# Kernel tuning notes

Measured on AMD Instinct MI355X. Metric: run time of the kernel, lower is better.

Reference implementation:

```python
import jax, jax.numpy as jnp
import numpy as np

NUM_CATEGORIES = 64
INPUT_DIM = 256
HIDDEN_DIM = 256
N = 4096  # number of samples (each with its own category)
M = 16    # rows per sample


def setup_inputs() -> dict:
    key = jax.random.key(0)
    k_x, k_cat, k_W = jax.random.split(key, 3)
    x = jax.random.normal(k_x, (N, M, INPUT_DIM), dtype=jnp.float32)
    cat_ids = jax.random.randint(k_cat, (N,), 0, NUM_CATEGORIES, dtype=jnp.int64)
    W = 0.02 * jax.random.normal(k_W, (NUM_CATEGORIES, INPUT_DIM, HIDDEN_DIM), dtype=jnp.float32)
    b = jnp.zeros((NUM_CATEGORIES, HIDDEN_DIM), dtype=jnp.float32)
    return {"x": x, "cat_ids": cat_ids, "W": W, "b": b}


def reference(x, cat_ids, W, b):
    # Gather per-sample weights/biases, then batched matmul + bias add.
    selected_W = W[cat_ids]              # [N, input_dim, hidden_dim]
    selected_b = b[cat_ids]              # [N, hidden_dim]
    out = jnp.einsum('nmi,nih->nmh', x, selected_W) + selected_b[:, None, :]
    return out
```

## Files before the change

kernel.cpp:

```cpp
#include <hip/hip_runtime.h>
#include <hip/hip_bf16.h>
#include <stdint.h>

#define N_SAMPLES 4096
#define M_ROWS 16
#define K_DIM 256
#define H_DIM 256
#define N_CATS 64
#define SPB 4
#define MAX_PADDED (N_SAMPLES + N_CATS * (SPB - 1))
#define NGROUP (MAX_PADDED / SPB)
#define GPX (NGROUP / 8)
#define GEMM_GRID (NGROUP * 2)
#define AROW 264

typedef _Float16 half8 __attribute__((ext_vector_type(8)));
typedef _Float16 half4 __attribute__((ext_vector_type(4)));
typedef float floatx4 __attribute__((ext_vector_type(4)));

#define WT_BYTES ((size_t)N_CATS * K_DIM * H_DIM * 2)
#define GCAT_OFF WT_BYTES
#define ORD_OFF  (WT_BYTES + 4288)
#define WS_NEED  (ORD_OFF + (size_t)MAX_PADDED * 4)

__global__ __launch_bounds__(256)
void prep_combined(const float* __restrict__ W, _Float16* __restrict__ Wt,
                   const int* __restrict__ cat, int* __restrict__ ord,
                   int* __restrict__ gcat) {
  const int tid = threadIdx.x;
  if (blockIdx.x < 1024) {
    __shared__ _Float16 t[64][72];
    const int bid = blockIdx.x;
    const int c  = bid >> 4;
    const int kb = (bid >> 2) & 3;
    const int hb = bid & 3;
    const int r  = tid >> 2;
    const int cg = (tid & 3) * 16;
    const float* src = W + ((size_t)c << 16) + (size_t)(kb * 64 + r) * 256 + hb * 64 + cg;
#pragma unroll
    for (int j = 0; j < 16; j += 4) {
      float4 v = *(const float4*)(src + j);
      t[r][cg + j + 0] = (_Float16)v.x;
      t[r][cg + j + 1] = (_Float16)v.y;
      t[r][cg + j + 2] = (_Float16)v.z;
      t[r][cg + j + 3] = (_Float16)v.w;
    }
    __syncthreads();
    _Float16* dst = Wt + ((size_t)c << 16) + (size_t)(hb * 64 + r) * 256 + kb * 64 + cg;
    half8 o0, o1;
#pragma unroll
    for (int j = 0; j < 8; j++) o0[j] = t[cg + j][r];
#pragma unroll
    for (int j = 0; j < 8; j++) o1[j] = t[cg + 8 + j][r];
    *(half8*)(dst) = o0;
    *(half8*)(dst + 8) = o1;
  } else {
    __shared__ int hist[N_CATS];
    __shared__ int poffs[N_CATS];
    __shared__ int curs[N_CATS];
    if (tid < N_CATS) hist[tid] = 0;
    for (int i = tid; i < MAX_PADDED; i += 256) ord[i] = -1;
    for (int i = tid; i < NGROUP; i += 256) gcat[i] = 0;
    __syncthreads();
    for (int i = tid; i < N_SAMPLES; i += 256) atomicAdd(&hist[cat[i]], 1);
    __syncthreads();
    if (tid == 0) {
      int run = 0;
      for (int c = 0; c < N_CATS; c++) {
        poffs[c] = run;
        run += ((hist[c] + SPB - 1) / SPB) * SPB;
      }
    }
    if (tid < N_CATS) curs[tid] = 0;
    __syncthreads();
    if (tid < N_CATS) {
      const int c = tid;
      const int g0 = poffs[c] >> 2;
      const int ng = (hist[c] + SPB - 1) >> 2;
      for (int g = 0; g < ng; g++) gcat[g0 + g] = c;
    }
    for (int i = tid; i < N_SAMPLES; i += 256) {
      int c = cat[i];
      int p = poffs[c] + atomicAdd(&curs[c], 1);
      ord[p] = i;
    }
  }
}

__global__ __launch_bounds__(256, 4)
void gemm_kernel(const float* __restrict__ x, const float* __restrict__ bias,
                 const _Float16* __restrict__ Wt, const int* __restrict__ ord,
                 const int* __restrict__ gcat, float* __restrict__ out) {
  __shared__ __align__(16) _Float16 sA[64 * AROW];

  const int tid = threadIdx.x;
  const int B = blockIdx.x;
  const int xcd = B & 7;
  const int slot = B >> 3;
  const int h_half = slot & 1;
  const int group = xcd * GPX + (slot >> 1);
  const int h0 = h_half << 7;

  const int cat = gcat[group];
  const int4 sm = *(const int4*)(ord + group * 4);
  if (sm.x < 0) return;

  const int wid  = tid >> 6;
  const int lane = tid & 63;
  const int l15  = lane & 15;
  const int quad = lane >> 4;

  const _Float16* wbase = Wt + ((size_t)cat << 16);

  half8 bf[8][2];
#pragma unroll
  for (int kt = 0; kt < 4; kt++)
#pragma unroll
    for (int nt = 0; nt < 2; nt++) {
      const int col = h0 + wid * 32 + nt * 16 + l15;
      bf[kt][nt] = *(const half8*)(wbase + (size_t)col * K_DIM + kt * 32 + quad * 8);
    }
  __builtin_amdgcn_sched_barrier(0);

  const int smp = (wid == 0) ? sm.x : (wid == 1) ? sm.y : (wid == 2) ? sm.z : sm.w;
  const float* asrc = (smp >= 0) ? (x + ((size_t)smp << 12)) : nullptr;
  _Float16* adst = sA + (size_t)(wid * 16) * AROW;
  if (asrc) {
#pragma unroll
    for (int j = 0; j < 16; j++) {
      float4 v = *(const float4*)(asrc + j * 256 + lane * 4);
      half4 h;
      h[0] = (_Float16)v.x; h[1] = (_Float16)v.y;
      h[2] = (_Float16)v.z; h[3] = (_Float16)v.w;
      *(half4*)(adst + (size_t)j * AROW + lane * 4) = h;
    }
  } else {
    half4 h;
#pragma unroll
    for (int e = 0; e < 4; e++) h[e] = (_Float16)0.0f;
#pragma unroll
    for (int j = 0; j < 16; j++)
      *(half4*)(adst + (size_t)j * AROW + lane * 4) = h;
  }

  floatx4 acc[4][2];
#pragma unroll
  for (int i = 0; i < 4; i++)
#pragma unroll
    for (int j = 0; j < 2; j++)
#pragma unroll
      for (int e = 0; e < 4; e++) acc[i][j][e] = 0.0f;

  __syncthreads();

#pragma unroll
  for (int kt = 0; kt < 8; kt++) {
    if (kt < 4) {
#pragma unroll
      for (int nt = 0; nt < 2; nt++) {
        const int col = h0 + wid * 32 + nt * 16 + l15;
        bf[kt + 4][nt] = *(const half8*)(wbase + (size_t)col * K_DIM + (kt + 4) * 32 + quad * 8);
      }
    }
    half8 af[4];
#pragma unroll
    for (int mt = 0; mt < 4; mt++)
      af[mt] = *(const half8*)&sA[(size_t)(mt * 16 + l15) * AROW + kt * 32 + quad * 8];
#pragma unroll
    for (int mt = 0; mt < 4; mt++)
#pragma unroll
      for (int nt = 0; nt < 2; nt++)
        acc[mt][nt] = __builtin_amdgcn_mfma_f32_16x16x32_f16(af[mt], bf[kt][nt], acc[mt][nt], 0, 0, 0);
  }

  float bv[2];
#pragma unroll
  for (int nt = 0; nt < 2; nt++)
    bv[nt] = bias[cat * H_DIM + h0 + wid * 32 + nt * 16 + l15];
  const int srow[4] = {sm.x, sm.y, sm.z, sm.w};
#pragma unroll
  for (int mt = 0; mt < 4; mt++) {
    const int s = srow[mt];
    if (s < 0) continue;
    float* obase = out + ((size_t)s << 12);
#pragma unroll
    for (int nt = 0; nt < 2; nt++) {
      const int col = h0 + wid * 32 + nt * 16 + l15;
#pragma unroll
      for (int rr = 0; rr < 4; rr++) {
        const int row = quad * 4 + rr;
        obase[(size_t)row * H_DIM + col] = acc[mt][nt][rr] + bv[nt];
      }
    }
  }
}

__global__ __launch_bounds__(256)
void naive_kernel(const float* __restrict__ x, const int* __restrict__ cat,
                  const float* __restrict__ W, const float* __restrict__ bias,
                  float* __restrict__ out) {
  __shared__ float sx[16 * 256];
  const int n = blockIdx.x;
  const int tid = threadIdx.x;
  const int c = cat[n];
  const float* xs = x + (size_t)n * 16 * 256;
  for (int i = tid; i < 16 * 256; i += 256) sx[i] = xs[i];
  __syncthreads();
  const float* Wc = W + ((size_t)c << 16);
  float accv[16];
  float bv = bias[c * 256 + tid];
#pragma unroll
  for (int m = 0; m < 16; m++) accv[m] = bv;
  for (int k = 0; k < 256; k++) {
    float w = Wc[(size_t)k * 256 + tid];
#pragma unroll
    for (int m = 0; m < 16; m++) accv[m] += sx[m * 256 + k] * w;
  }
#pragma unroll
  for (int m = 0; m < 16; m++) out[((size_t)n * 16 + m) * 256 + tid] = accv[m];
}

extern "C" void kernel_launch(void* const* d_in, const int* in_sizes, int n_in,
                              void* d_out, int out_size, void* d_ws, size_t ws_size,
                              hipStream_t stream) {
  const float* x    = (const float*)d_in[0];
  const int*   cat  = (const int*)d_in[1];
  const float* W    = (const float*)d_in[2];
  const float* bias = (const float*)d_in[3];
  float* out = (float*)d_out;

  if (ws_size < WS_NEED) {
    naive_kernel<<<N_SAMPLES, 256, 0, stream>>>(x, cat, W, bias, out);
    return;
  }

  char* ws = (char*)d_ws;
  _Float16* Wt = (_Float16*)ws;
  int* gcat = (int*)(ws + GCAT_OFF);
  int* ord  = (int*)(ws + ORD_OFF);

  prep_combined<<<1025, 256, 0, stream>>>(W, Wt, cat, ord, gcat);
  gemm_kernel<<<GEMM_GRID, 256, 0, stream>>>(x, bias, Wt, ord, gcat, out);
}
```

Before: 161.2 us.

## Use 512-thread blocks covering full hidden dim with XOR-swizzled LDS and ring-buffered B

Each block now handles one 4-sample group across all 256 hidden columns with 8 waves, instead of two blocks each covering half. The x tile is loaded and converted to fp16 once per group rather than twice. The padded LDS row layout is replaced by an XOR swizzle to avoid bank conflicts. The B-fragment prefetch shrinks from 8 to a 3-slot rotating buffer to cut register pressure at the higher occupancy target. The trade-off is half as many blocks and a shallower weight prefetch.

```diff
diff --git a/kernel.cpp b/kernel.cpp
--- a/kernel.cpp
+++ b/kernel.cpp
@@ -11,8 +11,6 @@
 #define MAX_PADDED (N_SAMPLES + N_CATS * (SPB - 1))
 #define NGROUP (MAX_PADDED / SPB)
 #define GPX (NGROUP / 8)
-#define GEMM_GRID (NGROUP * 2)
-#define AROW 264
 
 typedef _Float16 half8 __attribute__((ext_vector_type(8)));
 typedef _Float16 half4 __attribute__((ext_vector_type(4)));
@@ -87,19 +85,16 @@
   }
 }
 
-__global__ __launch_bounds__(256, 4)
+__global__ __launch_bounds__(512, 6)
 void gemm_kernel(const float* __restrict__ x, const float* __restrict__ bias,
                  const _Float16* __restrict__ Wt, const int* __restrict__ ord,
                  const int* __restrict__ gcat, float* __restrict__ out) {
-  __shared__ __align__(16) _Float16 sA[64 * AROW];
+  __shared__ __align__(16) _Float16 sA[64 * 256];
 
   const int tid = threadIdx.x;
   const int B = blockIdx.x;
   const int xcd = B & 7;
-  const int slot = B >> 3;
-  const int h_half = slot & 1;
-  const int group = xcd * GPX + (slot >> 1);
-  const int h0 = h_half << 7;
+  const int group = xcd * GPX + (B >> 3);
 
   const int cat = gcat[group];
   const int4 sm = *(const int4*)(ord + group * 4);
@@ -111,36 +106,39 @@
   const int quad = lane >> 4;
 
   const _Float16* wbase = Wt + ((size_t)cat << 16);
-
-  half8 bf[8][2];
-#pragma unroll
-  for (int kt = 0; kt < 4; kt++)
-#pragma unroll
-    for (int nt = 0; nt < 2; nt++) {
-      const int col = h0 + wid * 32 + nt * 16 + l15;
-      bf[kt][nt] = *(const half8*)(wbase + (size_t)col * K_DIM + kt * 32 + quad * 8);
-    }
+  const _Float16* bptr0 = wbase + (size_t)(wid * 32 + 0 * 16 + l15) * K_DIM + quad * 8;
+  const _Float16* bptr1 = wbase + (size_t)(wid * 32 + 1 * 16 + l15) * K_DIM + quad * 8;
+
+  half8 bf[3][2];
+#pragma unroll
+  for (int kt = 0; kt < 2; kt++) {
+    bf[kt][0] = *(const half8*)(bptr0 + kt * 32);
+    bf[kt][1] = *(const half8*)(bptr1 + kt * 32);
+  }
   __builtin_amdgcn_sched_barrier(0);
 
-  const int smp = (wid == 0) ? sm.x : (wid == 1) ? sm.y : (wid == 2) ? sm.z : sm.w;
-  const float* asrc = (smp >= 0) ? (x + ((size_t)smp << 12)) : nullptr;
-  _Float16* adst = sA + (size_t)(wid * 16) * AROW;
-  if (asrc) {
-#pragma unroll
-    for (int j = 0; j < 16; j++) {
-      float4 v = *(const float4*)(asrc + j * 256 + lane * 4);
+  const float* b0 = (sm.x >= 0) ? x + ((size_t)sm.x << 12) : nullptr;
+  const float* b1 = (sm.y >= 0) ? x + ((size_t)sm.y << 12) : nullptr;
+  const float* b2 = (sm.z >= 0) ? x + ((size_t)sm.z << 12) : nullptr;
+  const float* b3 = (sm.w >= 0) ? x + ((size_t)sm.w << 12) : nullptr;
+  const int wcol = (lane * 4) ^ (wid << 3);
+#pragma unroll
+  for (int i = 0; i < 8; i++) {
+    const float* bs = ((i >> 1) == 0) ? b0 : ((i >> 1) == 1) ? b1 : ((i >> 1) == 2) ? b2 : b3;
+    const int row = i * 8 + wid;
+    _Float16* adst = sA + row * 256 + wcol;
+    if (bs) {
+      float4 v = *(const float4*)(bs + (size_t)(((i & 1) * 8 + wid) * 256) + lane * 4);
       half4 h;
       h[0] = (_Float16)v.x; h[1] = (_Float16)v.y;
       h[2] = (_Float16)v.z; h[3] = (_Float16)v.w;
-      *(half4*)(adst + (size_t)j * AROW + lane * 4) = h;
-    }
-  } else {
-    half4 h;
-#pragma unroll
-    for (int e = 0; e < 4; e++) h[e] = (_Float16)0.0f;
-#pragma unroll
-    for (int j = 0; j < 16; j++)
-      *(half4*)(adst + (size_t)j * AROW + lane * 4) = h;
+      *(half4*)adst = h;
+    } else {
+      half4 h;
+#pragma unroll
+      for (int e = 0; e < 4; e++) h[e] = (_Float16)0.0f;
+      *(half4*)adst = h;
+    }
   }
 
   floatx4 acc[4][2];
@@ -153,30 +151,30 @@
 
   __syncthreads();
 
+  const int swz = (l15 & 7) << 3;
 #pragma unroll
   for (int kt = 0; kt < 8; kt++) {
-    if (kt < 4) {
-#pragma unroll
-      for (int nt = 0; nt < 2; nt++) {
-        const int col = h0 + wid * 32 + nt * 16 + l15;
-        bf[kt + 4][nt] = *(const half8*)(wbase + (size_t)col * K_DIM + (kt + 4) * 32 + quad * 8);
-      }
-    }
+    if (kt < 6) {
+      const int nx = (kt + 2) % 3;
+      bf[nx][0] = *(const half8*)(bptr0 + (kt + 2) * 32);
+      bf[nx][1] = *(const half8*)(bptr1 + (kt + 2) * 32);
+    }
+    const int cur = kt % 3;
     half8 af[4];
 #pragma unroll
     for (int mt = 0; mt < 4; mt++)
-      af[mt] = *(const half8*)&sA[(size_t)(mt * 16 + l15) * AROW + kt * 32 + quad * 8];
-#pragma unroll
-    for (int mt = 0; mt < 4; mt++)
-#pragma unroll
-      for (int nt = 0; nt < 2; nt++)
-        acc[mt][nt] = __builtin_amdgcn_mfma_f32_16x16x32_f16(af[mt], bf[kt][nt], acc[mt][nt], 0, 0, 0);
+      af[mt] = *(const half8*)&sA[(mt * 16 + l15) * 256 + ((kt * 32 + quad * 8) ^ swz)];
+#pragma unroll
+    for (int mt = 0; mt < 4; mt++) {
+      acc[mt][0] = __builtin_amdgcn_mfma_f32_16x16x32_f16(af[mt], bf[cur][0], acc[mt][0], 0, 0, 0);
+      acc[mt][1] = __builtin_amdgcn_mfma_f32_16x16x32_f16(af[mt], bf[cur][1], acc[mt][1], 0, 0, 0);
+    }
   }
 
   float bv[2];
 #pragma unroll
   for (int nt = 0; nt < 2; nt++)
-    bv[nt] = bias[cat * H_DIM + h0 + wid * 32 + nt * 16 + l15];
+    bv[nt] = bias[cat * H_DIM + wid * 32 + nt * 16 + l15];
   const int srow[4] = {sm.x, sm.y, sm.z, sm.w};
 #pragma unroll
   for (int mt = 0; mt < 4; mt++) {
@@ -185,7 +183,7 @@
     float* obase = out + ((size_t)s << 12);
 #pragma unroll
     for (int nt = 0; nt < 2; nt++) {
-      const int col = h0 + wid * 32 + nt * 16 + l15;
+      const int col = wid * 32 + nt * 16 + l15;
 #pragma unroll
       for (int rr = 0; rr < 4; rr++) {
         const int row = quad * 4 + rr;
@@ -240,5 +238,5 @@
   int* ord  = (int*)(ws + ORD_OFF);
 
   prep_combined<<<1025, 256, 0, stream>>>(W, Wt, cat, ord, gcat);
-  gemm_kernel<<<GEMM_GRID, 256, 0, stream>>>(x, bias, Wt, ord, gcat, out);
-}
+  gemm_kernel<<<NGROUP, 512, 0, stream>>>(x, bias, Wt, ord, gcat, out);
+}
```

New measurement: 166.6 us. 3.4% more time.

## Load A fragments directly from global into registers, double-buffered, dropping LDS staging

Applied to the files above, without the earlier changes.

The kernel no longer stages the x tile in shared memory. Each lane now loads its MFMA A-fragment straight from global memory as fp32, converts it to fp16 in registers, and double-buffers both the A and B fragments one k-step ahead. This removes the LDS writes and reads and the block barrier, with the goal of overlapping global loads with MFMA work. In exchange, x is read with less coalesced access (32-byte strided chunks per lane), register use rises so occupancy is lowered to 3, and each wave now reads the full x tile, so x is fetched four times per block instead of once.

```diff
diff --git a/kernel.cpp b/kernel.cpp
--- a/kernel.cpp
+++ b/kernel.cpp
@@ -12,7 +12,6 @@
 #define NGROUP (MAX_PADDED / SPB)
 #define GPX (NGROUP / 8)
 #define GEMM_GRID (NGROUP * 2)
-#define AROW 264
 
 typedef _Float16 half8 __attribute__((ext_vector_type(8)));
 typedef _Float16 half4 __attribute__((ext_vector_type(4)));
@@ -87,12 +86,38 @@
   }
 }
 
-__global__ __launch_bounds__(256, 4)
+#define ISSUE_A(NXT, ko)                                                         \
+  NXT[0][0] = *(const float4*)(a0 + (ko)); NXT[0][1] = *(const float4*)(a0 + (ko) + 4); \
+  NXT[1][0] = *(const float4*)(a1 + (ko)); NXT[1][1] = *(const float4*)(a1 + (ko) + 4); \
+  NXT[2][0] = *(const float4*)(a2 + (ko)); NXT[2][1] = *(const float4*)(a2 + (ko) + 4); \
+  NXT[3][0] = *(const float4*)(a3 + (ko)); NXT[3][1] = *(const float4*)(a3 + (ko) + 4);
+
+#define CVT_MFMA_ONE(CUR, mt, cb)                                                \
+  {                                                                              \
+    half8 af;                                                                    \
+    af[0] = (_Float16)CUR[mt][0].x; af[1] = (_Float16)CUR[mt][0].y;              \
+    af[2] = (_Float16)CUR[mt][0].z; af[3] = (_Float16)CUR[mt][0].w;              \
+    af[4] = (_Float16)CUR[mt][1].x; af[5] = (_Float16)CUR[mt][1].y;              \
+    af[6] = (_Float16)CUR[mt][1].z; af[7] = (_Float16)CUR[mt][1].w;              \
+    acc[mt][0] = __builtin_amdgcn_mfma_f32_16x16x32_f16(af, bf[cb][0], acc[mt][0], 0, 0, 0); \
+    acc[mt][1] = __builtin_amdgcn_mfma_f32_16x16x32_f16(af, bf[cb][1], acc[mt][1], 0, 0, 0); \
+  }
+
+#define KT_STEP(kt, CUR, NXT)                                                    \
+  if ((kt) < 7) { ISSUE_A(NXT, ((kt) + 1) * 32); }                               \
+  if ((kt) < 7) {                                                                \
+    bf[((kt) + 1) & 1][0] = *(const half8*)(wb + ((kt) + 1) * 32);               \
+    bf[((kt) + 1) & 1][1] = *(const half8*)(wb + 16 * K_DIM + ((kt) + 1) * 32);  \
+  }                                                                              \
+  CVT_MFMA_ONE(CUR, 0, (kt) & 1)                                                 \
+  CVT_MFMA_ONE(CUR, 1, (kt) & 1)                                                 \
+  CVT_MFMA_ONE(CUR, 2, (kt) & 1)                                                 \
+  CVT_MFMA_ONE(CUR, 3, (kt) & 1)
+
+__global__ __launch_bounds__(256, 3)
 void gemm_kernel(const float* __restrict__ x, const float* __restrict__ bias,
                  const _Float16* __restrict__ Wt, const int* __restrict__ ord,
                  const int* __restrict__ gcat, float* __restrict__ out) {
-  __shared__ __align__(16) _Float16 sA[64 * AROW];
-
   const int tid = threadIdx.x;
   const int B = blockIdx.x;
   const int xcd = B & 7;
@@ -105,43 +130,28 @@
   const int4 sm = *(const int4*)(ord + group * 4);
   if (sm.x < 0) return;
 
+  const int lane = tid & 63;
   const int wid  = tid >> 6;
-  const int lane = tid & 63;
   const int l15  = lane & 15;
   const int quad = lane >> 4;
 
-  const _Float16* wbase = Wt + ((size_t)cat << 16);
-
-  half8 bf[8][2];
-#pragma unroll
-  for (int kt = 0; kt < 4; kt++)
-#pragma unroll
-    for (int nt = 0; nt < 2; nt++) {
-      const int col = h0 + wid * 32 + nt * 16 + l15;
-      bf[kt][nt] = *(const half8*)(wbase + (size_t)col * K_DIM + kt * 32 + quad * 8);
-    }
-  __builtin_amdgcn_sched_barrier(0);
-
-  const int smp = (wid == 0) ? sm.x : (wid == 1) ? sm.y : (wid == 2) ? sm.z : sm.w;
-  const float* asrc = (smp >= 0) ? (x + ((size_t)smp << 12)) : nullptr;
-  _Float16* adst = sA + (size_t)(wid * 16) * AROW;
-  if (asrc) {
-#pragma unroll
-    for (int j = 0; j < 16; j++) {
-      float4 v = *(const float4*)(asrc + j * 256 + lane * 4);
-      half4 h;
-      h[0] = (_Float16)v.x; h[1] = (_Float16)v.y;
-      h[2] = (_Float16)v.z; h[3] = (_Float16)v.w;
-      *(half4*)(adst + (size_t)j * AROW + lane * 4) = h;
-    }
-  } else {
-    half4 h;
-#pragma unroll
-    for (int e = 0; e < 4; e++) h[e] = (_Float16)0.0f;
-#pragma unroll
-    for (int j = 0; j < 16; j++)
-      *(half4*)(adst + (size_t)j * AROW + lane * 4) = h;
-  }
+  const _Float16* wb = Wt + ((size_t)cat << 16) +
+                       (size_t)(h0 + wid * 32 + l15) * K_DIM + quad * 8;
+
+  const float* a0 = x + ((size_t)sm.x << 12) + l15 * 256 + quad * 8;
+  const float* a1 = x + ((size_t)(sm.y < 0 ? 0 : sm.y) << 12) + l15 * 256 + quad * 8;
+  const float* a2 = x + ((size_t)(sm.z < 0 ? 0 : sm.z) << 12) + l15 * 256 + quad * 8;
+  const float* a3 = x + ((size_t)(sm.w < 0 ? 0 : sm.w) << 12) + l15 * 256 + quad * 8;
+
+  half8 bf[2][2];
+  bf[0][0] = *(const half8*)(wb);
+  bf[0][1] = *(const half8*)(wb + 16 * K_DIM);
+
+  float4 arA[4][2], arB[4][2];
+  ISSUE_A(arA, 0);
+
+  const float bv0 = bias[cat * H_DIM + h0 + wid * 32 + l15];
+  const float bv1 = bias[cat * H_DIM + h0 + wid * 32 + 16 + l15];
 
   floatx4 acc[4][2];
 #pragma unroll
@@ -151,32 +161,15 @@
 #pragma unroll
       for (int e = 0; e < 4; e++) acc[i][j][e] = 0.0f;
 
-  __syncthreads();
-
-#pragma unroll
-  for (int kt = 0; kt < 8; kt++) {
-    if (kt < 4) {
-#pragma unroll
-      for (int nt = 0; nt < 2; nt++) {
-        const int col = h0 + wid * 32 + nt * 16 + l15;
-        bf[kt + 4][nt] = *(const half8*)(wbase + (size_t)col * K_DIM + (kt + 4) * 32 + quad * 8);
-      }
-    }
-    half8 af[4];
-#pragma unroll
-    for (int mt = 0; mt < 4; mt++)
-      af[mt] = *(const half8*)&sA[(size_t)(mt * 16 + l15) * AROW + kt * 32 + quad * 8];
-#pragma unroll
-    for (int mt = 0; mt < 4; mt++)
-#pragma unroll
-      for (int nt = 0; nt < 2; nt++)
-        acc[mt][nt] = __builtin_amdgcn_mfma_f32_16x16x32_f16(af[mt], bf[kt][nt], acc[mt][nt], 0, 0, 0);
-  }
-
-  float bv[2];
-#pragma unroll
-  for (int nt = 0; nt < 2; nt++)
-    bv[nt] = bias[cat * H_DIM + h0 + wid * 32 + nt * 16 + l15];
+  KT_STEP(0, arA, arB)
+  KT_STEP(1, arB, arA)
+  KT_STEP(2, arA, arB)
+  KT_STEP(3, arB, arA)
+  KT_STEP(4, arA, arB)
+  KT_STEP(5, arB, arA)
+  KT_STEP(6, arA, arB)
+  KT_STEP(7, arB, arA)
+
   const int srow[4] = {sm.x, sm.y, sm.z, sm.w};
 #pragma unroll
   for (int mt = 0; mt < 4; mt++) {
@@ -186,10 +179,11 @@
 #pragma unroll
     for (int nt = 0; nt < 2; nt++) {
       const int col = h0 + wid * 32 + nt * 16 + l15;
+      const float bv = nt ? bv1 : bv0;
 #pragma unroll
       for (int rr = 0; rr < 4; rr++) {
         const int row = quad * 4 + rr;
-        obase[(size_t)row * H_DIM + col] = acc[mt][nt][rr] + bv[nt];
+        obase[(size_t)row * H_DIM + col] = acc[mt][nt][rr] + bv;
       }
     }
   }
```

After: 220.6 us. +36.9%, slower.

## Compute both hidden halves per block to reuse staged A tile

Applied to the files above, without the earlier changes.

Each GEMM block now processes the full 256-wide hidden dimension in two sequential 128-column passes instead of splitting H across two blocks. The x tile is loaded and converted to fp16 in LDS once per group rather than twice, which halves x global reads and the conversion work. The first pass's tail prefetches the second half's weights, and the bias loads are hoisted. In exchange the grid is halved, so there is less parallelism and each block does serial work, and register pressure may rise.

```diff
diff --git a/kernel.cpp b/kernel.cpp
--- a/kernel.cpp
+++ b/kernel.cpp
@@ -11,7 +11,6 @@
 #define MAX_PADDED (N_SAMPLES + N_CATS * (SPB - 1))
 #define NGROUP (MAX_PADDED / SPB)
 #define GPX (NGROUP / 8)
-#define GEMM_GRID (NGROUP * 2)
 #define AROW 264
 
 typedef _Float16 half8 __attribute__((ext_vector_type(8)));
@@ -96,10 +95,7 @@
   const int tid = threadIdx.x;
   const int B = blockIdx.x;
   const int xcd = B & 7;
-  const int slot = B >> 3;
-  const int h_half = slot & 1;
-  const int group = xcd * GPX + (slot >> 1);
-  const int h0 = h_half << 7;
+  const int group = xcd * GPX + (B >> 3);
 
   const int cat = gcat[group];
   const int4 sm = *(const int4*)(ord + group * 4);
@@ -110,16 +106,21 @@
   const int l15  = lane & 15;
   const int quad = lane >> 4;
 
-  const _Float16* wbase = Wt + ((size_t)cat << 16);
+  const _Float16* wb0 = Wt + ((size_t)cat << 16) + (size_t)(wid * 32 + l15) * K_DIM + quad * 8;
+  const _Float16* wb1 = wb0 + (size_t)128 * K_DIM;
 
   half8 bf[8][2];
 #pragma unroll
-  for (int kt = 0; kt < 4; kt++)
-#pragma unroll
-    for (int nt = 0; nt < 2; nt++) {
-      const int col = h0 + wid * 32 + nt * 16 + l15;
-      bf[kt][nt] = *(const half8*)(wbase + (size_t)col * K_DIM + kt * 32 + quad * 8);
-    }
+  for (int kt = 0; kt < 4; kt++) {
+    bf[kt][0] = *(const half8*)(wb0 + kt * 32);
+    bf[kt][1] = *(const half8*)(wb0 + 16 * K_DIM + kt * 32);
+  }
+  float bv[2][2];
+#pragma unroll
+  for (int p = 0; p < 2; p++)
+#pragma unroll
+    for (int nt = 0; nt < 2; nt++)
+      bv[p][nt] = bias[cat * H_DIM + p * 128 + wid * 32 + nt * 16 + l15];
   __builtin_amdgcn_sched_barrier(0);
 
   const int smp = (wid == 0) ? sm.x : (wid == 1) ? sm.y : (wid == 2) ? sm.z : sm.w;
@@ -153,31 +154,28 @@
 
   __syncthreads();
 
+  const int srow[4] = {sm.x, sm.y, sm.z, sm.w};
+
 #pragma unroll
   for (int kt = 0; kt < 8; kt++) {
     if (kt < 4) {
-#pragma unroll
-      for (int nt = 0; nt < 2; nt++) {
-        const int col = h0 + wid * 32 + nt * 16 + l15;
-        bf[kt + 4][nt] = *(const half8*)(wbase + (size_t)col * K_DIM + (kt + 4) * 32 + quad * 8);
-      }
+      bf[kt + 4][0] = *(const half8*)(wb0 + (kt + 4) * 32);
+      bf[kt + 4][1] = *(const half8*)(wb0 + 16 * K_DIM + (kt + 4) * 32);
+    } else {
+      bf[kt - 4][0] = *(const half8*)(wb1 + (kt - 4) * 32);
+      bf[kt - 4][1] = *(const half8*)(wb1 + 16 * K_DIM + (kt - 4) * 32);
     }
     half8 af[4];
 #pragma unroll
     for (int mt = 0; mt < 4; mt++)
       af[mt] = *(const half8*)&sA[(size_t)(mt * 16 + l15) * AROW + kt * 32 + quad * 8];
 #pragma unroll
-    for (int mt = 0; mt < 4; mt++)
-#pragma unroll
-      for (int nt = 0; nt < 2; nt++)
-        acc[mt][nt] = __builtin_amdgcn_mfma_f32_16x16x32_f16(af[mt], bf[kt][nt], acc[mt][nt], 0, 0, 0);
-  }
-
-  float bv[2];
-#pragma unroll
-  for (int nt = 0; nt < 2; nt++)
-    bv[nt] = bias[cat * H_DIM + h0 + wid * 32 + nt * 16 + l15];
-  const int srow[4] = {sm.x, sm.y, sm.z, sm.w};
+    for (int mt = 0; mt < 4; mt++) {
+      acc[mt][0] = __builtin_amdgcn_mfma_f32_16x16x32_f16(af[mt], bf[kt][0], acc[mt][0], 0, 0, 0);
+      acc[mt][1] = __builtin_amdgcn_mfma_f32_16x16x32_f16(af[mt], bf[kt][1], acc[mt][1], 0, 0, 0);
+    }
+  }
+
 #pragma unroll
   for (int mt = 0; mt < 4; mt++) {
     const int s = srow[mt];
@@ -185,11 +183,51 @@
     float* obase = out + ((size_t)s << 12);
 #pragma unroll
     for (int nt = 0; nt < 2; nt++) {
-      const int col = h0 + wid * 32 + nt * 16 + l15;
+      const int col = wid * 32 + nt * 16 + l15;
 #pragma unroll
       for (int rr = 0; rr < 4; rr++) {
         const int row = quad * 4 + rr;
-        obase[(size_t)row * H_DIM + col] = acc[mt][nt][rr] + bv[nt];
+        obase[(size_t)row * H_DIM + col] = acc[mt][nt][rr] + bv[0][nt];
+      }
+    }
+  }
+
+#pragma unroll
+  for (int i = 0; i < 4; i++)
+#pragma unroll
+    for (int j = 0; j < 2; j++)
+#pragma unroll
+      for (int e = 0; e < 4; e++) acc[i][j][e] = 0.0f;
+
+#pragma unroll
+  for (int kt = 0; kt < 8; kt++) {
+    if (kt < 4) {
+      bf[kt + 4][0] = *(const half8*)(wb1 + (kt + 4) * 32);
+      bf[kt + 4][1] = *(const half8*)(wb1 + 16 * K_DIM + (kt + 4) * 32);
+    }
+    half8 af[4];
+#pragma unroll
+    for (int mt = 0; mt < 4; mt++)
+      af[mt] = *(const half8*)&sA[(size_t)(mt * 16 + l15) * AROW + kt * 32 + quad * 8];
+#pragma unroll
+    for (int mt = 0; mt < 4; mt++) {
+      acc[mt][0] = __builtin_amdgcn_mfma_f32_16x16x32_f16(af[mt], bf[kt][0], acc[mt][0], 0, 0, 0);
+      acc[mt][1] = __builtin_amdgcn_mfma_f32_16x16x32_f16(af[mt], bf[kt][1], acc[mt][1], 0, 0, 0);
+    }
+  }
+
+#pragma unroll
+  for (int mt = 0; mt < 4; mt++) {
+    const int s = srow[mt];
+    if (s < 0) continue;
+    float* obase = out + ((size_t)s << 12);
+#pragma unroll
+    for (int nt = 0; nt < 2; nt++) {
+      const int col = 128 + wid * 32 + nt * 16 + l15;
+#pragma unroll
+      for (int rr = 0; rr < 4; rr++) {
+        const int row = quad * 4 + rr;
+        obase[(size_t)row * H_DIM + col] = acc[mt][nt][rr] + bv[1][nt];
       }
     }
   }
@@ -240,5 +278,5 @@
   int* ord  = (int*)(ws + ORD_OFF);
 
   prep_combined<<<1025, 256, 0, stream>>>(W, Wt, cat, ord, gcat);
-  gemm_kernel<<<GEMM_GRID, 256, 0, stream>>>(x, bias, Wt, ord, gcat, out);
-}
+  gemm_kernel<<<NGROUP, 256, 0, stream>>>(x, bias, Wt, ord, gcat, out);
+}
```

After: 195.7 us. 1.21x slower.
